# Performance work log

Hardware: AMD Instinct MI355X
Metric: run time of the kernel (lower is better)

## Reference

```python
import jax, jax.numpy as jnp
import numpy as np

B, D, K = 32768, 256, 2048
BETA = 0.25


def setup_inputs() -> dict:
    key = jax.random.key(0)
    k1, k2 = jax.random.split(key)
    latents = jax.random.normal(k1, (B, D), dtype=jnp.float32)
    # nn.Embedding weight initialized uniform(-1/K, 1/K)
    embedding = jax.random.uniform(k2, (K, D), dtype=jnp.float32,
                                   minval=-1.0 / K, maxval=1.0 / K)
    return {"latents": latents, "embedding": embedding}


def reference(latents, embedding):
    # Squared-L2 distances: [B, K]
    dist = (jnp.sum(latents ** 2, axis=1, keepdims=True)
            + jnp.sum(embedding ** 2, axis=1)
            - 2.0 * jnp.matmul(latents, embedding.T))
    encoding_inds = jnp.argmin(dist, axis=1)  # [B]

    # Gather codebook rows (equivalent to one-hot @ embedding)
    quantized = embedding[encoding_inds]  # [B, D]

    commitment_loss = jnp.mean((jax.lax.stop_gradient(quantized) - latents) ** 2)
    embedding_loss = jnp.mean((quantized - jax.lax.stop_gradient(latents)) ** 2)
    vq_loss = commitment_loss * BETA + embedding_loss

    # Straight-through estimator
    quantized_st = latents + jax.lax.stop_gradient(quantized - latents)

    # avg_probs = mean of one-hot over batch == normalized histogram of inds
    counts = jnp.zeros((K,), dtype=jnp.float32).at[encoding_inds].add(1.0)
    avg_probs = counts / B
    entropy_vq = -jnp.sum(avg_probs * jnp.log(avg_probs + 1e-10))

    # dist values at selected codes
    cluster_metric = jnp.mean(
        jnp.take_along_axis(dist, encoding_inds[:, None], axis=1))

    return (quantized_st, vq_loss, entropy_vq,
            encoding_inds[:, None], cluster_metric)
```

## Files before the change

kernel.cpp:

```cpp
#include <hip/hip_runtime.h>
#include <math.h>

#define B_ROWS 32768
#define D_DIM  256
#define K_CODES 2048

#define OUT_Q   0
#define OUT_VQ  8388608
#define OUT_ENT 8388609
#define OUT_IND 8388610
#define OUT_CM  8421378


#define WS_SE2   0
#define WS_SX2   8192
#define WS_CNT   139264
#define WS_PACK  147456
#define WS_MSEP  409600
#define WS_DISTP 475136
#define WS_BCAT  540672

typedef _Float16 f16x8 __attribute__((ext_vector_type(8)));
typedef float f32x4 __attribute__((ext_vector_type(4)));
typedef union { _Float16 h[4]; uint2 u2; } h4pack;

__global__ __launch_bounds__(256) void k_convA(const float* __restrict__ X,
                                               _Float16* __restrict__ A,
                                               float* __restrict__ sx2) {
  int w = threadIdx.x >> 6, lane = threadIdx.x & 63;
  int row = blockIdx.x * 4 + w;
  float4 v = ((const float4*)(X + (size_t)row * D_DIM))[lane];
  float s = v.x * v.x + v.y * v.y + v.z * v.z + v.w * v.w;
#pragma unroll
  for (int off = 32; off > 0; off >>= 1) s += __shfl_xor(s, off, 64);
  if (lane == 0) sx2[row] = s;
  h4pack hi, lo;
  hi.h[0] = (_Float16)v.x; hi.h[1] = (_Float16)v.y;
  hi.h[2] = (_Float16)v.z; hi.h[3] = (_Float16)v.w;
  lo.h[0] = (_Float16)((v.x - (float)hi.h[0]) * 4096.0f);
  lo.h[1] = (_Float16)((v.y - (float)hi.h[1]) * 4096.0f);
  lo.h[2] = (_Float16)((v.z - (float)hi.h[2]) * 4096.0f);
  lo.h[3] = (_Float16)((v.w - (float)hi.h[3]) * 4096.0f);
  *(uint2*)&A[(size_t)row * 512 + 4 * lane] = hi.u2;
  *(uint2*)&A[(size_t)row * 512 + 256 + 4 * lane] = lo.u2;
}

__global__ __launch_bounds__(256) void k_convB(const float* __restrict__ E,
                                               _Float16* __restrict__ Bc,
                                               float* __restrict__ se2) {
  int w = threadIdx.x >> 6, lane = threadIdx.x & 63;
  int row = blockIdx.x * 4 + w;
  float4 v = ((const float4*)(E + (size_t)row * D_DIM))[lane];
  float s = v.x * v.x + v.y * v.y + v.z * v.z + v.w * v.w;
#pragma unroll
  for (int off = 32; off > 0; off >>= 1) s += __shfl_xor(s, off, 64);
  if (lane == 0) se2[row] = s;
  const float S = 4194304.0f;
  const float SH = 0.000244140625f;
  float e0 = v.x * S, e1 = v.y * S, e2 = v.z * S, e3 = v.w * S;
  h4pack b1, b2, b3;
  b1.h[0] = (_Float16)e0; b1.h[1] = (_Float16)e1;
  b1.h[2] = (_Float16)e2; b1.h[3] = (_Float16)e3;
  b2.h[0] = (_Float16)((float)b1.h[0] * SH);
  b2.h[1] = (_Float16)((float)b1.h[1] * SH);
  b2.h[2] = (_Float16)((float)b1.h[2] * SH);
  b2.h[3] = (_Float16)((float)b1.h[3] * SH);
  b3.h[0] = (_Float16)(e0 - (float)b1.h[0]);
  b3.h[1] = (_Float16)(e1 - (float)b1.h[1]);
  b3.h[2] = (_Float16)(e2 - (float)b1.h[2]);
  b3.h[3] = (_Float16)(e3 - (float)b1.h[3]);
  *(uint2*)&Bc[(size_t)row * 768 + 4 * lane] = b1.u2;
  *(uint2*)&Bc[(size_t)row * 768 + 256 + 4 * lane] = b2.u2;
  *(uint2*)&Bc[(size_t)row * 768 + 512 + 4 * lane] = b3.u2;
}

__global__ __launch_bounds__(256, 4) void k_mfma(
    const _Float16* __restrict__ A, const _Float16* __restrict__ Bc,
    const float* __restrict__ se2, const float* __restrict__ sx2,
    unsigned long long* __restrict__ packed) {
  __shared__ _Float16 As[2][128 * 32];
  __shared__ _Float16 Bs[2][128 * 32];
  __shared__ float sxs[128];
  const int tid = threadIdx.x;
  const int w = tid >> 6, lane = tid & 63;
  const int rowblk = blockIdx.x & 255, cg = blockIdx.x >> 8;
  const int row0 = rowblk * 128, col00 = cg * 512;
  const int lr = lane >> 2, lc = lane & 3;
  const int q = lane >> 4, c = lane & 15;
  const int wr = (w >> 1) * 64, wc = (w & 1) * 64;

  if (tid < 128) sxs[tid] = sx2[row0 + tid];

  const char* Abase = (const char*)A;
  const char* Bbase = (const char*)Bc;

  auto issue = [&](int ct_i, int ktl_i, int bsel) {
    int a_off = (ktl_i < 8) ? ktl_i * 64
              : (ktl_i < 16) ? 512 + (ktl_i - 8) * 64 : (ktl_i - 16) * 64;
    int b_off = ktl_i * 64;
    int colb = col00 + ct_i * 128;
#pragma unroll
    for (int t = 0; t < 2; ++t) {
      int s = w * 2 + t;
      const char* ga =
          Abase + (((size_t)(row0 + s * 16 + lr)) << 10) + a_off + lc * 16;
      const char* gb =
          Bbase + ((size_t)(colb + s * 16 + lr)) * 1536 + b_off + lc * 16;
      __builtin_amdgcn_global_load_lds(
          (const __attribute__((address_space(1))) unsigned int*)ga,
          (__attribute__((address_space(3))) unsigned int*)((char*)&As[bsel][0] +
                                                            s * 1024),
          16, 0, 0);
      __builtin_amdgcn_global_load_lds(
          (const __attribute__((address_space(1))) unsigned int*)gb,
          (__attribute__((address_space(3))) unsigned int*)((char*)&Bs[bsel][0] +
                                                            s * 1024),
          16, 0, 0);
    }
  };

  issue(0, 0, 0);

  const float inv = 4.76837158203125e-07f;
  for (int ct = 0; ct < 4; ++ct) {
    f32x4 acc[4][4];
#pragma unroll
    for (int i = 0; i < 4; i++)
#pragma unroll
      for (int j = 0; j < 4; j++) acc[i][j] = (f32x4){0.f, 0.f, 0.f, 0.f};

#pragma unroll 2
    for (int ktl = 0; ktl < 24; ++ktl) {
      __syncthreads();
      int gidx = ct * 24 + ktl + 1;
      if (gidx < 96) issue(gidx / 24, gidx % 24, (ktl + 1) & 1);
      const int b = ktl & 1;
      f16x8 af[4], bf[4];
#pragma unroll
      for (int i = 0; i < 4; ++i) {
        af[i] = *(const f16x8*)&As[b][(wr + i * 16 + c) * 32 + q * 8];
        bf[i] = *(const f16x8*)&Bs[b][(wc + i * 16 + c) * 32 + q * 8];
      }
#pragma unroll
      for (int i = 0; i < 4; ++i)
#pragma unroll
        for (int j = 0; j < 4; ++j)
          acc[i][j] = __builtin_amdgcn_mfma_f32_16x16x32_f16(af[i], bf[j],
                                                             acc[i][j], 0, 0, 0);
    }

    int colb = col00 + ct * 128;
    float se_j[4];
#pragma unroll
    for (int j = 0; j < 4; ++j) se_j[j] = se2[colb + wc + j * 16 + c];
#pragma unroll
    for (int i = 0; i < 4; ++i) {
#pragma unroll
      for (int r = 0; r < 4; ++r) {
        int lrow = wr + i * 16 + q * 4 + r;
        float sx = sxs[lrow];
        float bs = 3.402823466e38f;
        int bk = 0;
#pragma unroll
        for (int j = 0; j < 4; ++j) {
          float t1 = sx + se_j[j];
          float d = t1 - acc[i][j][r] * inv;
          if (d < bs) { bs = d; bk = colb + wc + j * 16 + c; }
        }
#pragma unroll
        for (int off = 1; off < 16; off <<= 1) {
          float os = __shfl_xor(bs, off, 64);
          int ok = __shfl_xor(bk, off, 64);
          if (os < bs || (os == bs && ok < bk)) { bs = os; bk = ok; }
        }
        if (c == 0) {
          unsigned long long v =
              ((unsigned long long)__float_as_uint(bs) << 32) |
              (unsigned long long)(unsigned int)bk;
          atomicMin(&packed[row0 + lrow], v);
        }
      }
    }
  }
}

__global__ __launch_bounds__(256) void k_gather(
    const float* __restrict__ X, const float* __restrict__ E,
    const unsigned long long* __restrict__ packed, float* __restrict__ outq,
    float* __restrict__ out_ind, int* __restrict__ counts,
    double* __restrict__ msep, double* __restrict__ distp) {
  __shared__ int sk[16];
  __shared__ float sd[16];
  int tid = threadIdx.x;
  if (tid < 16) {
    int row = blockIdx.x * 16 + tid;
    unsigned long long v = packed[row];
    int k = (int)(v & 0xFFFFFFFFull);
    sk[tid] = k;
    sd[tid] = __uint_as_float((unsigned int)(v >> 32));
    out_ind[row] = (float)k;
    atomicAdd(&counts[k], 1);
  }
  __syncthreads();
  int wave = tid >> 6, lane = tid & 63;
  double msum = 0.0, dsum = 0.0;
#pragma unroll
  for (int rr = 0; rr < 4; rr++) {
    int li = wave * 4 + rr;
    int b = blockIdx.x * 16 + li;
    int ind = sk[li];
    float4 x4 = ((const float4*)(X + (size_t)b * D_DIM))[lane];
    float4 q4 = ((const float4*)(E + (size_t)ind * D_DIM))[lane];
    float d0 = q4.x - x4.x, d1 = q4.y - x4.y, d2 = q4.z - x4.z, d3 = q4.w - x4.w;
    float4 o;
    o.x = x4.x + d0; o.y = x4.y + d1; o.z = x4.z + d2; o.w = x4.w + d3;
    ((float4*)(outq + (size_t)b * D_DIM))[lane] = o;
    float v = d0 * d0 + d1 * d1 + d2 * d2 + d3 * d3;
#pragma unroll
    for (int off = 32; off > 0; off >>= 1) v += __shfl_xor(v, off, 64);
    if (lane == 0) { msum += (double)v; dsum += (double)sd[li]; }
  }
  if (lane == 0) {
    int wg = blockIdx.x * 4 + wave;
    msep[wg] = msum;
    distp[wg] = dsum;
  }
}

__global__ __launch_bounds__(256) void k_final(
    const int* __restrict__ counts, const double* __restrict__ msep,
    const double* __restrict__ distp, float* __restrict__ out) {
  __shared__ double red[256];
  int t = threadIdx.x;

  double m = 0.0;
  for (int i = t; i < 8192; i += 256) m += msep[i];
  red[t] = m;
  __syncthreads();
  for (int s = 128; s > 0; s >>= 1) {
    if (t < s) red[t] += red[t + s];
    __syncthreads();
  }
  if (t == 0) {
    double mse = red[0] / ((double)B_ROWS * (double)D_DIM);
    out[OUT_VQ] = (float)(mse * 1.25);
  }
  __syncthreads();

  double d = 0.0;
  for (int i = t; i < 8192; i += 256) d += distp[i];
  red[t] = d;
  __syncthreads();
  for (int s = 128; s > 0; s >>= 1) {
    if (t < s) red[t] += red[t + s];
    __syncthreads();
  }
  if (t == 0) out[OUT_CM] = (float)(red[0] / (double)B_ROWS);
  __syncthreads();

  double e = 0.0;
  for (int k = t; k < K_CODES; k += 256) {
    float p = (float)counts[k] * (1.0f / 32768.0f);
    e += (double)(p * logf(p + 1e-10f));
  }
  red[t] = e;
  __syncthreads();
  for (int s = 128; s > 0; s >>= 1) {
    if (t < s) red[t] += red[t + s];
    __syncthreads();
  }
  if (t == 0) out[OUT_ENT] = (float)(-red[0]);
}

extern "C" void kernel_launch(void* const* d_in, const int* in_sizes, int n_in,
                              void* d_out, int out_size, void* d_ws,
                              size_t ws_size, hipStream_t stream) {
  const float* X = (const float*)d_in[0];
  const float* E = (const float*)d_in[1];
  float* out = (float*)d_out;
  char* ws = (char*)d_ws;
  float* se2 = (float*)(ws + WS_SE2);
  float* sx2 = (float*)(ws + WS_SX2);
  int* counts = (int*)(ws + WS_CNT);
  unsigned long long* packed = (unsigned long long*)(ws + WS_PACK);
  double* msep = (double*)(ws + WS_MSEP);
  double* distp = (double*)(ws + WS_DISTP);
  _Float16* Bcat = (_Float16*)(ws + WS_BCAT);
  _Float16* Acat = (_Float16*)d_out;

  hipMemsetAsync(counts, 0, K_CODES * sizeof(int), stream);
  hipMemsetAsync(packed, 0xFF, B_ROWS * sizeof(unsigned long long), stream);
  k_convA<<<B_ROWS / 4, 256, 0, stream>>>(X, Acat, sx2);
  k_convB<<<K_CODES / 4, 256, 0, stream>>>(E, Bcat, se2);
  k_mfma<<<1024, 256, 0, stream>>>(Acat, Bcat, se2, sx2, packed);
  k_gather<<<B_ROWS / 16, 256, 0, stream>>>(X, E, packed, out + OUT_Q,
                                            out + OUT_IND, counts, msep, distp);
  k_final<<<1, 256, 0, stream>>>(counts, msep, distp, out);
}
```

Before: 277.0 us.

## Fuse conversion and init into one kernel, double MFMA grid, keep row norms in registers

Merges the two fp16-split conversion kernels and the two memsets into a single k_init launch, with the workspace initialisation (packed sentinel, zeroed counts) done inside it. Each MFMA block now covers 256 instead of 512 codebook columns, so the grid doubles to 2048 blocks for more parallelism, at the cost of twice as many atomic argmin merges per row. Row squared norms are now loaded straight into registers as float4 instead of being staged in shared memory. The aim is to cut launch overhead and to balance the GPU better.

```diff
diff --git a/kernel.cpp b/kernel.cpp
--- a/kernel.cpp
+++ b/kernel.cpp
@@ -24,54 +24,55 @@
 typedef float f32x4 __attribute__((ext_vector_type(4)));
 typedef union { _Float16 h[4]; uint2 u2; } h4pack;
 
-__global__ __launch_bounds__(256) void k_convA(const float* __restrict__ X,
-                                               _Float16* __restrict__ A,
-                                               float* __restrict__ sx2) {
+__global__ __launch_bounds__(256) void k_init(
+    const float* __restrict__ X, const float* __restrict__ E,
+    _Float16* __restrict__ A, _Float16* __restrict__ Bc,
+    float* __restrict__ sx2, float* __restrict__ se2,
+    unsigned long long* __restrict__ packed, int* __restrict__ counts) {
   int w = threadIdx.x >> 6, lane = threadIdx.x & 63;
-  int row = blockIdx.x * 4 + w;
-  float4 v = ((const float4*)(X + (size_t)row * D_DIM))[lane];
-  float s = v.x * v.x + v.y * v.y + v.z * v.z + v.w * v.w;
-#pragma unroll
-  for (int off = 32; off > 0; off >>= 1) s += __shfl_xor(s, off, 64);
-  if (lane == 0) sx2[row] = s;
-  h4pack hi, lo;
-  hi.h[0] = (_Float16)v.x; hi.h[1] = (_Float16)v.y;
-  hi.h[2] = (_Float16)v.z; hi.h[3] = (_Float16)v.w;
-  lo.h[0] = (_Float16)((v.x - (float)hi.h[0]) * 4096.0f);
-  lo.h[1] = (_Float16)((v.y - (float)hi.h[1]) * 4096.0f);
-  lo.h[2] = (_Float16)((v.z - (float)hi.h[2]) * 4096.0f);
-  lo.h[3] = (_Float16)((v.w - (float)hi.h[3]) * 4096.0f);
-  *(uint2*)&A[(size_t)row * 512 + 4 * lane] = hi.u2;
-  *(uint2*)&A[(size_t)row * 512 + 256 + 4 * lane] = lo.u2;
-}
-
-__global__ __launch_bounds__(256) void k_convB(const float* __restrict__ E,
-                                               _Float16* __restrict__ Bc,
-                                               float* __restrict__ se2) {
-  int w = threadIdx.x >> 6, lane = threadIdx.x & 63;
-  int row = blockIdx.x * 4 + w;
-  float4 v = ((const float4*)(E + (size_t)row * D_DIM))[lane];
-  float s = v.x * v.x + v.y * v.y + v.z * v.z + v.w * v.w;
-#pragma unroll
-  for (int off = 32; off > 0; off >>= 1) s += __shfl_xor(s, off, 64);
-  if (lane == 0) se2[row] = s;
-  const float S = 4194304.0f;
-  const float SH = 0.000244140625f;
-  float e0 = v.x * S, e1 = v.y * S, e2 = v.z * S, e3 = v.w * S;
-  h4pack b1, b2, b3;
-  b1.h[0] = (_Float16)e0; b1.h[1] = (_Float16)e1;
-  b1.h[2] = (_Float16)e2; b1.h[3] = (_Float16)e3;
-  b2.h[0] = (_Float16)((float)b1.h[0] * SH);
-  b2.h[1] = (_Float16)((float)b1.h[1] * SH);
-  b2.h[2] = (_Float16)((float)b1.h[2] * SH);
-  b2.h[3] = (_Float16)((float)b1.h[3] * SH);
-  b3.h[0] = (_Float16)(e0 - (float)b1.h[0]);
-  b3.h[1] = (_Float16)(e1 - (float)b1.h[1]);
-  b3.h[2] = (_Float16)(e2 - (float)b1.h[2]);
-  b3.h[3] = (_Float16)(e3 - (float)b1.h[3]);
-  *(uint2*)&Bc[(size_t)row * 768 + 4 * lane] = b1.u2;
-  *(uint2*)&Bc[(size_t)row * 768 + 256 + 4 * lane] = b2.u2;
-  *(uint2*)&Bc[(size_t)row * 768 + 512 + 4 * lane] = b3.u2;
+  if (blockIdx.x < 8192) {
+    int row = blockIdx.x * 4 + w;
+    float4 v = ((const float4*)(X + (size_t)row * D_DIM))[lane];
+    float s = v.x * v.x + v.y * v.y + v.z * v.z + v.w * v.w;
+#pragma unroll
+    for (int off = 32; off > 0; off >>= 1) s += __shfl_xor(s, off, 64);
+    if (lane == 0) { sx2[row] = s; packed[row] = ~0ull; }
+    h4pack hi, lo;
+    hi.h[0] = (_Float16)v.x; hi.h[1] = (_Float16)v.y;
+    hi.h[2] = (_Float16)v.z; hi.h[3] = (_Float16)v.w;
+    lo.h[0] = (_Float16)((v.x - (float)hi.h[0]) * 4096.0f);
+    lo.h[1] = (_Float16)((v.y - (float)hi.h[1]) * 4096.0f);
+    lo.h[2] = (_Float16)((v.z - (float)hi.h[2]) * 4096.0f);
+    lo.h[3] = (_Float16)((v.w - (float)hi.h[3]) * 4096.0f);
+    *(uint2*)&A[(size_t)row * 512 + 4 * lane] = hi.u2;
+    *(uint2*)&A[(size_t)row * 512 + 256 + 4 * lane] = lo.u2;
+  } else {
+    int bb = blockIdx.x - 8192;
+    int row = bb * 4 + w;
+    if (threadIdx.x < 4) counts[bb * 4 + threadIdx.x] = 0;
+    float4 v = ((const float4*)(E + (size_t)row * D_DIM))[lane];
+    float s = v.x * v.x + v.y * v.y + v.z * v.z + v.w * v.w;
+#pragma unroll
+    for (int off = 32; off > 0; off >>= 1) s += __shfl_xor(s, off, 64);
+    if (lane == 0) se2[row] = s;
+    const float S = 4194304.0f;
+    const float SH = 0.000244140625f;
+    float e0 = v.x * S, e1 = v.y * S, e2 = v.z * S, e3 = v.w * S;
+    h4pack b1, b2, b3;
+    b1.h[0] = (_Float16)e0; b1.h[1] = (_Float16)e1;
+    b1.h[2] = (_Float16)e2; b1.h[3] = (_Float16)e3;
+    b2.h[0] = (_Float16)((float)b1.h[0] * SH);
+    b2.h[1] = (_Float16)((float)b1.h[1] * SH);
+    b2.h[2] = (_Float16)((float)b1.h[2] * SH);
+    b2.h[3] = (_Float16)((float)b1.h[3] * SH);
+    b3.h[0] = (_Float16)(e0 - (float)b1.h[0]);
+    b3.h[1] = (_Float16)(e1 - (float)b1.h[1]);
+    b3.h[2] = (_Float16)(e2 - (float)b1.h[2]);
+    b3.h[3] = (_Float16)(e3 - (float)b1.h[3]);
+    *(uint2*)&Bc[(size_t)row * 768 + 4 * lane] = b1.u2;
+    *(uint2*)&Bc[(size_t)row * 768 + 256 + 4 * lane] = b2.u2;
+    *(uint2*)&Bc[(size_t)row * 768 + 512 + 4 * lane] = b3.u2;
+  }
 }
 
 __global__ __launch_bounds__(256, 4) void k_mfma(
@@ -80,16 +81,18 @@
     unsigned long long* __restrict__ packed) {
   __shared__ _Float16 As[2][128 * 32];
   __shared__ _Float16 Bs[2][128 * 32];
-  __shared__ float sxs[128];
   const int tid = threadIdx.x;
   const int w = tid >> 6, lane = tid & 63;
   const int rowblk = blockIdx.x & 255, cg = blockIdx.x >> 8;
-  const int row0 = rowblk * 128, col00 = cg * 512;
+  const int row0 = rowblk * 128, col00 = cg * 256;
   const int lr = lane >> 2, lc = lane & 3;
   const int q = lane >> 4, c = lane & 15;
   const int wr = (w >> 1) * 64, wc = (w & 1) * 64;
 
-  if (tid < 128) sxs[tid] = sx2[row0 + tid];
+  float4 srow[4];
+#pragma unroll
+  for (int i = 0; i < 4; ++i)
+    srow[i] = *(const float4*)&sx2[row0 + wr + i * 16 + q * 4];
 
   const char* Abase = (const char*)A;
   const char* Bbase = (const char*)Bc;
@@ -122,7 +125,7 @@
   issue(0, 0, 0);
 
   const float inv = 4.76837158203125e-07f;
-  for (int ct = 0; ct < 4; ++ct) {
+  for (int ct = 0; ct < 2; ++ct) {
     f32x4 acc[4][4];
 #pragma unroll
     for (int i = 0; i < 4; i++)
@@ -133,7 +136,7 @@
     for (int ktl = 0; ktl < 24; ++ktl) {
       __syncthreads();
       int gidx = ct * 24 + ktl + 1;
-      if (gidx < 96) issue(gidx / 24, gidx % 24, (ktl + 1) & 1);
+      if (gidx < 48) issue(gidx / 24, gidx % 24, (ktl + 1) & 1);
       const int b = ktl & 1;
       f16x8 af[4], bf[4];
 #pragma unroll
@@ -158,7 +161,7 @@
 #pragma unroll
       for (int r = 0; r < 4; ++r) {
         int lrow = wr + i * 16 + q * 4 + r;
-        float sx = sxs[lrow];
+        float sx = ((const float*)&srow[i])[r];
         float bs = 3.402823466e38f;
         int bk = 0;
 #pragma unroll
@@ -288,11 +291,8 @@
   _Float16* Bcat = (_Float16*)(ws + WS_BCAT);
   _Float16* Acat = (_Float16*)d_out;
 
-  hipMemsetAsync(counts, 0, K_CODES * sizeof(int), stream);
-  hipMemsetAsync(packed, 0xFF, B_ROWS * sizeof(unsigned long long), stream);
-  k_convA<<<B_ROWS / 4, 256, 0, stream>>>(X, Acat, sx2);
-  k_convB<<<K_CODES / 4, 256, 0, stream>>>(E, Bcat, se2);
-  k_mfma<<<1024, 256, 0, stream>>>(Acat, Bcat, se2, sx2, packed);
+  k_init<<<8704, 256, 0, stream>>>(X, E, Acat, Bcat, sx2, se2, packed, counts);
+  k_mfma<<<2048, 256, 0, stream>>>(Acat, Bcat, se2, sx2, packed);
   k_gather<<<B_ROWS / 16, 256, 0, stream>>>(X, E, packed, out + OUT_Q,
                                             out + OUT_IND, counts, msep, distp);
   k_final<<<1, 256, 0, stream>>>(counts, msep, distp, out);
```

Measured after the change: 272.1 us. Within noise of the previous version (-1.8%).
